# Performance work log

Measured on AMD Instinct MI355X. Metric: run time of the kernel, lower is better.

## Reference

```python
import jax, jax.numpy as jnp
import numpy as np

PAD = 2
EPS = 1e-5


def setup_inputs() -> dict:
    key = jax.random.key(0)
    k1, = jax.random.split(key, 1)
    N, C, H, W = 32, 64, 224, 224
    x = jax.random.normal(k1, (N, C, H, W), dtype=jnp.float32)
    bn_weight = jnp.ones((C,), dtype=jnp.float32)
    bn_bias = jnp.zeros((C,), dtype=jnp.float32)
    post_scale = jnp.asarray(0.5, dtype=jnp.float32)
    return {"x": x, "bn_weight": bn_weight, "bn_bias": bn_bias, "post_scale": post_scale}


def reference(x, bn_weight, bn_bias, post_scale):
    # 1) reflection pad H and W by PAD on each side -> (N, C, H+2p, W+2p)
    pad_x = jnp.pad(x, ((0, 0), (0, 0), (PAD, PAD), (PAD, PAD)), mode="reflect")
    # 2-4) GLU over [pad_x, roll(pad_x)] along channels == pad_x * sigmoid(roll)
    pad_x_roll = jnp.roll(pad_x, shift=1, axis=1)
    gated = pad_x * jax.nn.sigmoid(pad_x_roll)
    # 5) global average pool -> (N, C)
    pooled = gated.mean(axis=(2, 3))
    # 6) BatchNorm1d (training mode: batch stats, biased variance, affine)
    mu = pooled.mean(axis=0)
    var = pooled.var(axis=0)  # biased, matches BN normalization
    normed = (pooled - mu) / jnp.sqrt(var + EPS) * bn_weight + bn_bias
    # 7-9) sigmoid reweight + channel-mean residual + scalar scale + exact GELU
    scale = jax.nn.sigmoid(normed)[:, :, None, None]
    channel_mean = pad_x.mean(axis=(2, 3), keepdims=True)
    out = jax.nn.gelu((gated * scale + channel_mean) * post_scale, approximate=False)
    return out.reshape(out.shape[0], -1)
```

## Files before the change

kernel.cpp:

```cpp
#include <hip/hip_runtime.h>
#include <math.h>

#define NB 32
#define CB 64
#define HH 224
#define WW 224
#define PADP 2
#define HP (HH + 2*PADP)
#define WP (WW + 2*PADP)
#define HW (HH*WW)
#define HWP (HP*WP)
#define EPSV 1e-5f
#define CHUNKS 49

typedef float v4f __attribute__((ext_vector_type(4)));

__device__ __forceinline__ float fsig(float v) {
    float e = __expf(-v);
    return __builtin_amdgcn_rcpf(1.0f + e);
}
__device__ __forceinline__ float fgelu(float v) {
    float t = v * (1.5957691216f + 0.0713548162f * v * v);
    return v * fsig(t);
}
__device__ __forceinline__ float edgew(int w) {
    return 1.0f + (float)((w == 1) | (w == 2) | (w == WW-3) | (w == WW-2));
}

__global__ __launch_bounds__(256) void k_pool3(const float* __restrict__ x,
                                               float* __restrict__ partG,
                                               float* __restrict__ partX) {
    int b = blockIdx.x;
    int n = b / CHUNKS;
    int chunk = b - n * CHUNKS;
    int wave = threadIdx.x >> 6;
    int lane = threadIdx.x & 63;

    int p0 = chunk * 1024 + lane * 4;
    float4 wgt[4];
    #pragma unroll
    for (int m = 0; m < 4; ++m) {
        int pm = p0 + m * 256;
        int h  = pm / WW;
        int w0 = pm - h * WW;
        float wh = 1.0f + (float)((h == 1) | (h == 2) | (h == HH-3) | (h == HH-2));
        wgt[m].x = wh * edgew(w0);
        wgt[m].y = wh * edgew(w0 + 1);
        wgt[m].z = wh * edgew(w0 + 2);
        wgt[m].w = wh * edgew(w0 + 3);
    }

    const float* xn = x + (size_t)n * CB * HW;
    int c0 = wave * 16;
    int cg = (c0 + CB - 1) & (CB - 1);
    float4 prev[4];
    #pragma unroll
    for (int m = 0; m < 4; ++m)
        prev[m] = *(const float4*)(xn + (size_t)cg * HW + p0 + m * 256);

    for (int k = 0; k < 16; ++k) {
        int c = c0 + k;
        float4 cur[4];
        #pragma unroll
        for (int m = 0; m < 4; ++m)
            cur[m] = *(const float4*)(xn + (size_t)c * HW + p0 + m * 256);
        float sG = 0.f, sX = 0.f;
        #pragma unroll
        for (int m = 0; m < 4; ++m) {
            sG += wgt[m].x * cur[m].x * fsig(prev[m].x);
            sG += wgt[m].y * cur[m].y * fsig(prev[m].y);
            sG += wgt[m].z * cur[m].z * fsig(prev[m].z);
            sG += wgt[m].w * cur[m].w * fsig(prev[m].w);
            sX += wgt[m].x * cur[m].x + wgt[m].y * cur[m].y
                + wgt[m].z * cur[m].z + wgt[m].w * cur[m].w;
            prev[m] = cur[m];
        }
        #pragma unroll
        for (int off = 32; off >= 1; off >>= 1) {
            sG += __shfl_xor(sG, off);
            sX += __shfl_xor(sX, off);
        }
        if (lane == 0) {
            size_t idx = ((size_t)n * CB + c) * CHUNKS + chunk;
            partG[idx] = sG;
            partX[idx] = sX;
        }
    }
}

__global__ __launch_bounds__(256) void k_stats(const float* __restrict__ partG,
                                               const float* __restrict__ partX,
                                               const float* __restrict__ bnw,
                                               const float* __restrict__ bnb,
                                               float* __restrict__ cmean,
                                               float* __restrict__ scale) {
    int c = blockIdx.x;
    int t = threadIdx.x;
    int n = t >> 3, j0 = t & 7;
    float g = 0.f, xx = 0.f;
    for (int j = j0; j < CHUNKS; j += 8) {
        size_t idx = ((size_t)n * CB + c) * CHUNKS + j;
        g  += partG[idx];
        xx += partX[idx];
    }
    #pragma unroll
    for (int off = 4; off >= 1; off >>= 1) {
        g  += __shfl_xor(g, off);
        xx += __shfl_xor(xx, off);
    }
    __shared__ float lG[NB];
    if (j0 == 0) {
        lG[n] = g;
        cmean[n * CB + c] = xx * (1.0f / (float)HWP);
    }
    __syncthreads();
    if (t < NB) {
        float p = lG[t] * (1.0f / (float)HWP);
        float s = p;
        #pragma unroll
        for (int off = 16; off >= 1; off >>= 1) s += __shfl_xor(s, off);
        float mu = s * (1.0f / 32.0f);
        float d = p - mu;
        float q = d * d;
        #pragma unroll
        for (int off = 16; off >= 1; off >>= 1) q += __shfl_xor(q, off);
        float var = q * (1.0f / 32.0f);
        float normed = d * rsqrtf(var + EPSV) * bnw[c] + bnb[c];
        scale[t * CB + c] = 1.0f / (1.0f + expf(-normed));
    }
}

__global__ __launch_bounds__(256) void k_out(const float* __restrict__ x,
                                             const float* __restrict__ scale,
                                             const float* __restrict__ cmean,
                                             const float* __restrict__ post_scale,
                                             float* __restrict__ out) {
    int o = blockIdx.x;
    int w = (o & 7) * (NB * HP / 8) + (o >> 3);
    int n  = w / HP;
    int hp = w - n * HP;
    int rh = hp - PADP; rh = rh < 0 ? -rh : (rh >= HH ? 2*HH - 2 - rh : rh);
    int wave = threadIdx.x >> 6;
    int lane = threadIdx.x & 63;
    bool act = lane < 56;
    float ps = post_scale[0];

    const float* xrow = x + (size_t)n * CB * HW + (size_t)rh * WW;
    const float* sc_row = scale + n * CB;
    const float* cm_row = cmean + n * CB;

    int c0 = wave * 16;
    int cg = (c0 + CB - 1) & (CB - 1);
    v4f prev = {0.f, 0.f, 0.f, 0.f};
    if (act) prev = __builtin_nontemporal_load((const v4f*)(xrow + (size_t)cg * HW + 4 * lane));

    for (int k = 0; k < 16; ++k) {
        int c = c0 + k;
        v4f cur = {0.f, 0.f, 0.f, 0.f};
        if (act) cur = __builtin_nontemporal_load((const v4f*)(xrow + (size_t)c * HW + 4 * lane));
        float scp = sc_row[c] * ps;
        float cmp = cm_row[c] * ps;
        float o0 = fgelu(fmaf(cur.x * fsig(prev.x), scp, cmp));
        float o1 = fgelu(fmaf(cur.y * fsig(prev.y), scp, cmp));
        float o2 = fgelu(fmaf(cur.z * fsig(prev.z), scp, cmp));
        float o3 = fgelu(fmaf(cur.w * fsig(prev.w), scp, cmp));
        float o1s = __shfl(o1, lane - 1);
        float o2s = __shfl(o2, lane - 1);
        float o3s = __shfl(o3, lane - 1);
        v4f st = { o2s, o3s, o0, o1 };
        if (lane == 0)  st = (v4f){ o2, o1, o0, o1 };
        if (lane == 56) st = (v4f){ o2s, o3s, o2s, o1s };
        if (lane < 57) {
            float* orow = out + ((size_t)n * CB + c) * HWP + (size_t)hp * WP;
            __builtin_nontemporal_store(st, (v4f*)(orow + 4 * lane));
        }
        prev = cur;
    }
}

extern "C" void kernel_launch(void* const* d_in, const int* in_sizes, int n_in,
                              void* d_out, int out_size, void* d_ws, size_t ws_size,
                              hipStream_t stream) {
    const float* x   = (const float*)d_in[0];
    const float* bnw = (const float*)d_in[1];
    const float* bnb = (const float*)d_in[2];
    const float* ps  = (const float*)d_in[3];
    float* out = (float*)d_out;

    size_t npart = (size_t)NB * CB * CHUNKS;
    float* partG  = (float*)d_ws;
    float* partX  = partG + npart;
    float* cmean  = partX + npart;
    float* scale  = cmean + NB * CB;

    k_pool3<<<NB * CHUNKS, 256, 0, stream>>>(x, partG, partX);
    k_stats<<<CB, 256, 0, stream>>>(partG, partX, bnw, bnb, cmean, scale);
    k_out<<<NB * HP, 256, 0, stream>>>(x, scale, cmean, ps, out);
}
```

Baseline: 253.1 us.

## Split work by spatial position per wave and loop all channels in-wave

The pooling kernel now gives each wave a distinct 256-pixel slice and has it walk all 64 channels, instead of splitting channels across waves. Per-wave partials are combined through shared memory before the global write, and loads are nontemporal. The output kernel likewise gives each wave its own padded row (4 rows per block) over all channels, so each block handles four rows. This cuts the redundant rolled-channel halo loads and changes the memory access pattern, but gives each wave a longer serial channel loop with fewer independent loads in flight.

Result: slower. 267.0 us (+5.5%).

```diff
diff --git a/kernel.cpp b/kernel.cpp
--- a/kernel.cpp
+++ b/kernel.cpp
@@ -12,6 +12,7 @@
 #define HWP (HP*WP)
 #define EPSV 1e-5f
 #define CHUNKS 49
+#define GROUPS 57
 
 typedef float v4f __attribute__((ext_vector_type(4)));
 
@@ -27,7 +28,7 @@
     return 1.0f + (float)((w == 1) | (w == 2) | (w == WW-3) | (w == WW-2));
 }
 
-__global__ __launch_bounds__(256) void k_pool3(const float* __restrict__ x,
+__global__ __launch_bounds__(256) void k_pool4(const float* __restrict__ x,
                                                float* __restrict__ partG,
                                                float* __restrict__ partX) {
     int b = blockIdx.x;
@@ -36,55 +37,42 @@
     int wave = threadIdx.x >> 6;
     int lane = threadIdx.x & 63;
 
-    int p0 = chunk * 1024 + lane * 4;
-    float4 wgt[4];
-    #pragma unroll
-    for (int m = 0; m < 4; ++m) {
-        int pm = p0 + m * 256;
-        int h  = pm / WW;
-        int w0 = pm - h * WW;
-        float wh = 1.0f + (float)((h == 1) | (h == 2) | (h == HH-3) | (h == HH-2));
-        wgt[m].x = wh * edgew(w0);
-        wgt[m].y = wh * edgew(w0 + 1);
-        wgt[m].z = wh * edgew(w0 + 2);
-        wgt[m].w = wh * edgew(w0 + 3);
-    }
+    int p0 = chunk * 1024 + wave * 256 + lane * 4;
+    int h  = p0 / WW;
+    int w0 = p0 - h * WW;
+    float wh = 1.0f + (float)((h == 1) | (h == 2) | (h == HH-3) | (h == HH-2));
+    float wg0 = wh * edgew(w0);
+    float wg1 = wh * edgew(w0 + 1);
+    float wg2 = wh * edgew(w0 + 2);
+    float wg3 = wh * edgew(w0 + 3);
 
     const float* xn = x + (size_t)n * CB * HW;
-    int c0 = wave * 16;
-    int cg = (c0 + CB - 1) & (CB - 1);
-    float4 prev[4];
-    #pragma unroll
-    for (int m = 0; m < 4; ++m)
-        prev[m] = *(const float4*)(xn + (size_t)cg * HW + p0 + m * 256);
+    v4f prev = __builtin_nontemporal_load((const v4f*)(xn + (size_t)(CB-1) * HW + p0));
 
-    for (int k = 0; k < 16; ++k) {
-        int c = c0 + k;
-        float4 cur[4];
-        #pragma unroll
-        for (int m = 0; m < 4; ++m)
-            cur[m] = *(const float4*)(xn + (size_t)c * HW + p0 + m * 256);
-        float sG = 0.f, sX = 0.f;
-        #pragma unroll
-        for (int m = 0; m < 4; ++m) {
-            sG += wgt[m].x * cur[m].x * fsig(prev[m].x);
-            sG += wgt[m].y * cur[m].y * fsig(prev[m].y);
-            sG += wgt[m].z * cur[m].z * fsig(prev[m].z);
-            sG += wgt[m].w * cur[m].w * fsig(prev[m].w);
-            sX += wgt[m].x * cur[m].x + wgt[m].y * cur[m].y
-                + wgt[m].z * cur[m].z + wgt[m].w * cur[m].w;
-            prev[m] = cur[m];
-        }
+    __shared__ float lG[4][CB];
+    __shared__ float lX[4][CB];
+
+    for (int c = 0; c < CB; ++c) {
+        v4f cur = __builtin_nontemporal_load((const v4f*)(xn + (size_t)c * HW + p0));
+        float sG = wg0 * cur.x * fsig(prev.x)
+                 + wg1 * cur.y * fsig(prev.y)
+                 + wg2 * cur.z * fsig(prev.z)
+                 + wg3 * cur.w * fsig(prev.w);
+        float sX = wg0 * cur.x + wg1 * cur.y + wg2 * cur.z + wg3 * cur.w;
         #pragma unroll
         for (int off = 32; off >= 1; off >>= 1) {
             sG += __shfl_xor(sG, off);
             sX += __shfl_xor(sX, off);
         }
-        if (lane == 0) {
-            size_t idx = ((size_t)n * CB + c) * CHUNKS + chunk;
-            partG[idx] = sG;
-            partX[idx] = sX;
-        }
+        if (lane == 0) { lG[wave][c] = sG; lX[wave][c] = sX; }
+        prev = cur;
+    }
+    __syncthreads();
+    if (threadIdx.x < 128) {
+        int c = threadIdx.x & 63, which = threadIdx.x >> 6;
+        size_t idx = ((size_t)n * CB + c) * CHUNKS + chunk;
+        if (which == 0) partG[idx] = lG[0][c] + lG[1][c] + lG[2][c] + lG[3][c];
+        else            partX[idx] = lX[0][c] + lX[1][c] + lX[2][c] + lX[3][c];
     }
 }
 
@@ -130,18 +118,19 @@
     }
 }
 
-__global__ __launch_bounds__(256) void k_out(const float* __restrict__ x,
-                                             const float* __restrict__ scale,
-                                             const float* __restrict__ cmean,
-                                             const float* __restrict__ post_scale,
-                                             float* __restrict__ out) {
+__global__ __launch_bounds__(256) void k_out2(const float* __restrict__ x,
+                                              const float* __restrict__ scale,
+                                              const float* __restrict__ cmean,
+                                              const float* __restrict__ post_scale,
+                                              float* __restrict__ out) {
     int o = blockIdx.x;
-    int w = (o & 7) * (NB * HP / 8) + (o >> 3);
-    int n  = w / HP;
-    int hp = w - n * HP;
-    int rh = hp - PADP; rh = rh < 0 ? -rh : (rh >= HH ? 2*HH - 2 - rh : rh);
+    int b = (o & 7) * (NB * GROUPS / 8) + (o >> 3);
+    int n = b / GROUPS;
+    int g = b - n * GROUPS;
     int wave = threadIdx.x >> 6;
     int lane = threadIdx.x & 63;
+    int hp = g * 4 + wave;
+    int rh = hp - PADP; rh = rh < 0 ? -rh : (rh >= HH ? 2*HH - 2 - rh : rh);
     bool act = lane < 56;
     float ps = post_scale[0];
 
@@ -149,13 +138,10 @@
     const float* sc_row = scale + n * CB;
     const float* cm_row = cmean + n * CB;
 
-    int c0 = wave * 16;
-    int cg = (c0 + CB - 1) & (CB - 1);
     v4f prev = {0.f, 0.f, 0.f, 0.f};
-    if (act) prev = __builtin_nontemporal_load((const v4f*)(xrow + (size_t)cg * HW + 4 * lane));
+    if (act) prev = __builtin_nontemporal_load((const v4f*)(xrow + (size_t)(CB-1) * HW + 4 * lane));
 
-    for (int k = 0; k < 16; ++k) {
-        int c = c0 + k;
+    for (int c = 0; c < CB; ++c) {
         v4f cur = {0.f, 0.f, 0.f, 0.f};
         if (act) cur = __builtin_nontemporal_load((const v4f*)(xrow + (size_t)c * HW + 4 * lane));
         float scp = sc_row[c] * ps;
@@ -193,7 +179,7 @@
     float* cmean  = partX + npart;
     float* scale  = cmean + NB * CB;
 
-    k_pool3<<<NB * CHUNKS, 256, 0, stream>>>(x, partG, partX);
+    k_pool4<<<NB * CHUNKS, 256, 0, stream>>>(x, partG, partX);
     k_stats<<<CB, 256, 0, stream>>>(partG, partX, bnw, bnb, cmean, scale);
-    k_out<<<NB * HP, 256, 0, stream>>>(x, scale, cmean, ps, out);
+    k_out2<<<NB * GROUPS, 256, 0, stream>>>(x, scale, cmean, ps, out);
 }
```
